# Kernel optimization log

Measured on AMD Instinct MI355X. Metric: run time of the kernel, lower is better.

The kernel has to match this reference:

```python
import jax, jax.numpy as jnp
import numpy as np

B, S, D, H, E = 4, 2048, 2048, 4096, 8
TOP_K = 2
ENTROPY_WEIGHT = 0.1
MAX_USAGE_RATIO = 0.3


def setup_inputs() -> dict:
    key = jax.random.key(0)
    k0, k1, k2 = jax.random.split(key, 3)
    x = jax.random.normal(k0, (B, S, D), dtype=jnp.float32)
    gate_w = jax.random.normal(k1, (E, D), dtype=jnp.float32) * 0.02
    gate_b = jnp.zeros((E,), dtype=jnp.float32)
    expert_w = jax.random.normal(k2, (E, H, D), dtype=jnp.float32) * 0.02
    expert_b = jnp.zeros((E, H), dtype=jnp.float32)
    return {"x": x, "gate_w": gate_w, "gate_b": gate_b,
            "expert_w": expert_w, "expert_b": expert_b}


def reference(x, gate_w, gate_b, expert_w, expert_b):
    b, s, d = x.shape
    e, h, _ = expert_w.shape
    n = b * s
    xf = x.reshape(n, d)

    # gating
    gate_logits = xf @ gate_w.T + gate_b              # (N, E)
    gate_probs = jax.nn.softmax(gate_logits, axis=-1)
    entropy = (-jnp.sum(gate_probs * jnp.log(gate_probs + 1e-10), axis=-1)).mean()
    entropy_loss = ENTROPY_WEIGHT * entropy

    # top-k dispatch weights
    topk_probs, topk_idx = jax.lax.top_k(gate_probs, TOP_K)   # (N, K)
    combine = jnp.sum(jax.nn.one_hot(topk_idx, e, dtype=xf.dtype)
                      * topk_probs[..., None], axis=1)        # (N, E)

    # per-expert linear + weighted combine (loop over small fixed E)
    out = jnp.zeros((n, h), dtype=xf.dtype)
    for ei in range(e):
        out = out + combine[:, ei:ei + 1] * (xf @ expert_w[ei].T + expert_b[ei])

    # usage penalty (this batch's routing counts)
    counts = jnp.sum(jax.nn.one_hot(topk_idx, e, dtype=jnp.float32), axis=(0, 1))
    usage_ratios = counts / n
    overuse_penalty = jnp.sum(jax.nn.relu(usage_ratios - MAX_USAGE_RATIO))

    return out.reshape(b, s, h), entropy_loss + overuse_penalty
```

## Files before the change

### kernel.cpp

```cpp
#include <hip/hip_runtime.h>

constexpr int N_TOK = 8192;
constexpr int D_IN  = 2048;
constexpr int H_OUT = 4096;
constexpr int NEXP  = 8;
constexpr float ENT_W = 0.1f;
constexpr float MAX_USAGE = 0.3f;

constexpr int TM = 128;
constexpr int TH = 128;
constexpr int BK = 32;
constexpr int NKT = D_IN / BK;
constexpr int TILES_H = H_OUT / TH;
constexpr int TM_MAX  = N_TOK / TM;
constexpr int REGION  = 8192;
constexpr int BUFSZ   = TM * BK;

typedef __attribute__((ext_vector_type(8))) short bf16x8;
typedef __attribute__((ext_vector_type(4))) float f32x4;

__device__ __forceinline__ short f2bf(float f) {
    unsigned u = __float_as_uint(f);
    u += 0x7FFF + ((u >> 16) & 1);
    return (short)(u >> 16);
}

__device__ __forceinline__ void gload16(const void* g, void* l) {
    __builtin_amdgcn_global_load_lds(
        (const __attribute__((address_space(1))) unsigned int*)g,
        (__attribute__((address_space(3))) unsigned int*)l, 16, 0, 0);
}

__global__ __launch_bounds__(256) void cvt_kernel(
    const float* __restrict__ in, short* __restrict__ out, int n8)
{
    int stride = gridDim.x * 256;
    for (int i = blockIdx.x * 256 + threadIdx.x; i < n8; i += stride) {
        const float4* p = (const float4*)in + (size_t)i * 2;
        float4 a = p[0], b = p[1];
        bf16x8 v;
        v[0] = f2bf(a.x); v[1] = f2bf(a.y); v[2] = f2bf(a.z); v[3] = f2bf(a.w);
        v[4] = f2bf(b.x); v[5] = f2bf(b.y); v[6] = f2bf(b.z); v[7] = f2bf(b.w);
        *(bf16x8*)(out + (size_t)i * 8) = v;
    }
}

__global__ __launch_bounds__(256) void gate_kernel(
    const float* __restrict__ x, const float* __restrict__ gate_w,
    const float* __restrict__ gate_b, int* __restrict__ topk_idx,
    float* __restrict__ topk_w, float* __restrict__ ent_partial,
    short* __restrict__ xb)
{
    __shared__ float ent_s[4];
    const int wv = threadIdx.x >> 6;
    const int lane = threadIdx.x & 63;
    const int t = blockIdx.x * 4 + wv;

    float acc[NEXP];
#pragma unroll
    for (int e = 0; e < NEXP; ++e) acc[e] = 0.f;

    const float4* xr = (const float4*)(x + (size_t)t * D_IN);
    short* xbr = xb + (size_t)t * D_IN;
#pragma unroll
    for (int i = 0; i < D_IN / 256; ++i) {
        float4 xv = xr[lane + i * 64];
        short4 s4;
        s4.x = f2bf(xv.x); s4.y = f2bf(xv.y); s4.z = f2bf(xv.z); s4.w = f2bf(xv.w);
        *(short4*)(xbr + i * 256 + lane * 4) = s4;
#pragma unroll
        for (int e = 0; e < NEXP; ++e) {
            float4 gv = ((const float4*)(gate_w + e * D_IN))[lane + i * 64];
            acc[e] += xv.x * gv.x + xv.y * gv.y + xv.z * gv.z + xv.w * gv.w;
        }
    }
#pragma unroll
    for (int e = 0; e < NEXP; ++e)
#pragma unroll
        for (int m = 32; m >= 1; m >>= 1) acc[e] += __shfl_xor(acc[e], m, 64);

    if (lane == 0) {
        float lg[NEXP], p[NEXP];
        float mx = -1e30f;
#pragma unroll
        for (int e = 0; e < NEXP; ++e) { lg[e] = acc[e] + gate_b[e]; mx = fmaxf(mx, lg[e]); }
        float s = 0.f;
#pragma unroll
        for (int e = 0; e < NEXP; ++e) { p[e] = expf(lg[e] - mx); s += p[e]; }
        float inv = 1.f / s;
        float ent = 0.f;
#pragma unroll
        for (int e = 0; e < NEXP; ++e) { p[e] *= inv; ent -= p[e] * logf(p[e] + 1e-10f); }
        int e1 = 0; float b1 = p[0];
#pragma unroll
        for (int e = 1; e < NEXP; ++e) if (p[e] > b1) { b1 = p[e]; e1 = e; }
        int e2 = (e1 == 0) ? 1 : 0; float b2 = p[e2];
#pragma unroll
        for (int e = 0; e < NEXP; ++e)
            if (e != e1 && e != ((e1 == 0) ? 1 : 0) && p[e] > b2) { b2 = p[e]; e2 = e; }
        topk_idx[2 * t]     = e1;  topk_idx[2 * t + 1] = e2;
        topk_w[2 * t]       = b1;  topk_w[2 * t + 1]   = b2;
        ent_s[wv] = ent;
    }
    __syncthreads();
    if (threadIdx.x == 0)
        ent_partial[blockIdx.x] = ent_s[0] + ent_s[1] + ent_s[2] + ent_s[3];
}

__global__ __launch_bounds__(256) void scatter_kernel(
    const int* __restrict__ topk_idx, const float* __restrict__ topk_w,
    int* __restrict__ cursors, int* __restrict__ tok_list,
    float* __restrict__ w_list)
{
    __shared__ int lcnt[NEXP], lbase[NEXP];
    const int tid = threadIdx.x;
    const int t = blockIdx.x * 256 + tid;
    if (tid < NEXP) lcnt[tid] = 0;
    __syncthreads();
    int e0 = topk_idx[2 * t], e1 = topk_idx[2 * t + 1];
    float w0 = topk_w[2 * t], w1 = topk_w[2 * t + 1];
    int p0 = atomicAdd(&lcnt[e0], 1);
    int p1 = atomicAdd(&lcnt[e1], 1);
    __syncthreads();
    if (tid < NEXP) lbase[tid] = atomicAdd(&cursors[tid], lcnt[tid]);
    __syncthreads();
    int d0 = e0 * REGION + lbase[e0] + p0;
    int d1 = e1 * REGION + lbase[e1] + p1;
    tok_list[d0] = t;  w_list[d0] = w0;
    tok_list[d1] = t;  w_list[d1] = w1;
}

__global__ __launch_bounds__(256) void finalize_kernel(
    const int* __restrict__ counts, const float* __restrict__ ent_partial,
    float* __restrict__ loss_out)
{
    __shared__ float red[256];
    float s = 0.f;
    for (int i = threadIdx.x; i < N_TOK / 4; i += 256) s += ent_partial[i];
    red[threadIdx.x] = s;
    __syncthreads();
    for (int st = 128; st > 0; st >>= 1) {
        if (threadIdx.x < st) red[threadIdx.x] += red[threadIdx.x + st];
        __syncthreads();
    }
    if (threadIdx.x == 0) {
        float loss = ENT_W * red[0] / (float)N_TOK;
        for (int e = 0; e < NEXP; ++e) {
            float r = (float)counts[e] / (float)N_TOK - MAX_USAGE;
            if (r > 0.f) loss += r;
        }
        loss_out[0] = loss;
    }
}

__global__ __launch_bounds__(256, 4) void moe_gemm(
    const short* __restrict__ xb, const short* __restrict__ wb,
    const float* __restrict__ expert_b, const int* __restrict__ tok_list,
    const float* __restrict__ w_list, const int* __restrict__ counts,
    float* __restrict__ out)
{
    const int bid = blockIdx.x;
    const int e   = bid / (TM_MAX * TILES_H);
    const int rem = bid % (TM_MAX * TILES_H);
    const int tm  = rem / TILES_H;
    const int th  = rem % TILES_H;

    const int cnt = counts[e];
    if (tm * TM >= cnt) return;
    const int valid = cnt - tm * TM;
    const int hbase = th * TH;

    __shared__ __align__(16) short A_s[2][BUFSZ];
    __shared__ __align__(16) short B_s[2][BUFSZ];
    __shared__ int   tok_s[TM];
    __shared__ float wgt_s[TM];

    const int tid = threadIdx.x;
    if (tid < TM) {
        bool v = tid < valid;
        int src = e * REGION + tm * TM + tid;
        tok_s[tid] = v ? tok_list[src] : 0;
        wgt_s[tid] = v ? w_list[src] : 0.f;
    }
    __syncthreads();

    const int lane = tid & 63;
    const int wv = tid >> 6;

    const char* asrc[2];
    const char* bsrc[2];
    int dst_off[2];
#pragma unroll
    for (int j = 0; j < 2; ++j) {
        int c = wv * 2 + j;
        int r = c * 16 + (lane >> 2);
        int s2 = (lane & 3) ^ ((lane >> 3) & 3);
        asrc[j] = (const char*)(xb + (size_t)tok_s[r] * D_IN) + s2 * 16;
        bsrc[j] = (const char*)(wb + ((size_t)e * H_OUT + hbase + r) * D_IN) + s2 * 16;
        dst_off[j] = c * 512;
    }

    const int rr = lane & 15, kg = lane >> 4;
    const int wr = wv >> 1, wc = wv & 1;

    int aoff[4], boff[4];
#pragma unroll
    for (int mi = 0; mi < 4; ++mi) {
        int row = wr * 64 + mi * 16 + rr;
        aoff[mi] = row * 32 + (kg ^ ((row >> 1) & 3)) * 8;
        int rowb = wc * 64 + mi * 16 + rr;
        boff[mi] = rowb * 32 + (kg ^ ((rowb >> 1) & 3)) * 8;
    }

    f32x4 acc[4][4] = {};

#pragma unroll
    for (int j = 0; j < 2; ++j) {
        gload16(asrc[j], (short*)A_s[0] + dst_off[j]); asrc[j] += BK * 2;
        gload16(bsrc[j], (short*)B_s[0] + dst_off[j]); bsrc[j] += BK * 2;
    }
#pragma unroll
    for (int j = 0; j < 2; ++j) {
        gload16(asrc[j], (short*)A_s[1] + dst_off[j]); asrc[j] += BK * 2;
        gload16(bsrc[j], (short*)B_s[1] + dst_off[j]); bsrc[j] += BK * 2;
    }
    asm volatile("s_waitcnt vmcnt(4)" ::: "memory");
    __builtin_amdgcn_sched_barrier(0);
    __builtin_amdgcn_s_barrier();

    for (int kt = 0; kt < NKT; ++kt) {
        const short* Ac = A_s[kt & 1];
        const short* Bc = B_s[kt & 1];
        short* An = (short*)A_s[kt & 1];
        short* Bn = (short*)B_s[kt & 1];

        bf16x8 af[4], bv[4];
#pragma unroll
        for (int mi = 0; mi < 4; ++mi) af[mi] = *(const bf16x8*)&Ac[aoff[mi]];
#pragma unroll
        for (int ni = 0; ni < 4; ++ni) bv[ni] = *(const bf16x8*)&Bc[boff[ni]];
        asm volatile("s_waitcnt lgkmcnt(0)" ::: "memory");
        __builtin_amdgcn_sched_barrier(0);
        __builtin_amdgcn_s_barrier();

        if (kt + 2 < NKT) {
#pragma unroll
            for (int j = 0; j < 2; ++j) {
                gload16(asrc[j], An + dst_off[j]); asrc[j] += BK * 2;
                gload16(bsrc[j], Bn + dst_off[j]); bsrc[j] += BK * 2;
            }
        }

        __builtin_amdgcn_s_setprio(1);
#pragma unroll
        for (int mi = 0; mi < 4; ++mi)
#pragma unroll
            for (int ni = 0; ni < 4; ++ni)
                acc[mi][ni] = __builtin_amdgcn_mfma_f32_16x16x32_bf16(
                    af[mi], bv[ni], acc[mi][ni], 0, 0, 0);
        __builtin_amdgcn_s_setprio(0);

        if (kt + 2 < NKT) {
            asm volatile("s_waitcnt vmcnt(4)" ::: "memory");
        } else if (kt + 1 < NKT) {
            asm volatile("s_waitcnt vmcnt(0)" ::: "memory");
        }
        __builtin_amdgcn_sched_barrier(0);
        __builtin_amdgcn_s_barrier();
    }

    const float* bias = expert_b + (size_t)e * H_OUT + hbase;
#pragma unroll
    for (int mi = 0; mi < 4; ++mi) {
#pragma unroll
        for (int ni = 0; ni < 4; ++ni) {
            int col = wc * 64 + ni * 16 + rr;
            float be = bias[col];
#pragma unroll
            for (int i = 0; i < 4; ++i) {
                int r = wr * 64 + mi * 16 + kg * 4 + i;
                if (r < valid) {
                    float val = wgt_s[r] * (acc[mi][ni][i] + be);
                    atomicAdd(&out[(size_t)tok_s[r] * H_OUT + hbase + col], val);
                }
            }
        }
    }
}

extern "C" void kernel_launch(void* const* d_in, const int* in_sizes, int n_in,
                              void* d_out, int out_size, void* d_ws, size_t ws_size,
                              hipStream_t stream) {
    const float* x        = (const float*)d_in[0];
    const float* gate_w   = (const float*)d_in[1];
    const float* gate_b   = (const float*)d_in[2];
    const float* expert_w = (const float*)d_in[3];
    const float* expert_b = (const float*)d_in[4];
    float* out = (float*)d_out;
    char* ws = (char*)d_ws;

    int*   topk_idx    = (int*)(ws);
    float* topk_w      = (float*)(ws + (64 << 10));
    int*   cursors     = (int*)(ws + (128 << 10));
    float* ent_partial = (float*)(ws + (128 << 10) + 256);
    int*   tok_list    = (int*)(ws + (160 << 10));
    float* w_list      = (float*)(ws + (416 << 10));
    short* xb          = (short*)(ws + (1ull << 20));
    short* wb          = (short*)(ws + (34ull << 20));

    hipMemsetAsync(cursors, 0, 64, stream);
    hipMemsetAsync(d_out, 0, (size_t)out_size * sizeof(float), stream);

    gate_kernel<<<N_TOK / 4, 256, 0, stream>>>(x, gate_w, gate_b, topk_idx,
                                               topk_w, ent_partial, xb);
    cvt_kernel<<<4096, 256, 0, stream>>>(expert_w, wb, (NEXP * H_OUT * D_IN) / 8);
    scatter_kernel<<<N_TOK / 256, 256, 0, stream>>>(topk_idx, topk_w, cursors,
                                                    tok_list, w_list);
    finalize_kernel<<<1, 256, 0, stream>>>(cursors, ent_partial,
                                           out + (size_t)N_TOK * H_OUT);
    moe_gemm<<<NEXP * TM_MAX * TILES_H, 256, 0, stream>>>(
        xb, wb, expert_b, tok_list, w_list, cursors, out);
}
```

Before: 665.0 us.

## Enlarge MoE GEMM tile to 256x128x64 with 512 threads and triple-buffered LDS

```diff
diff --git a/kernel.cpp b/kernel.cpp
--- a/kernel.cpp
+++ b/kernel.cpp
@@ -7,14 +7,15 @@
 constexpr float ENT_W = 0.1f;
 constexpr float MAX_USAGE = 0.3f;
 
-constexpr int TM = 128;
-constexpr int TH = 128;
-constexpr int BK = 32;
+constexpr int BM = 256;
+constexpr int BN = 128;
+constexpr int BK = 64;
 constexpr int NKT = D_IN / BK;
-constexpr int TILES_H = H_OUT / TH;
-constexpr int TM_MAX  = N_TOK / TM;
+constexpr int TILES_H = H_OUT / BN;
+constexpr int TILES_M = N_TOK / BM;
 constexpr int REGION  = 8192;
-constexpr int BUFSZ   = TM * BK;
+constexpr int ASLOT = BM * BK;
+constexpr int BSLOT = BN * BK;
 
 typedef __attribute__((ext_vector_type(8))) short bf16x8;
 typedef __attribute__((ext_vector_type(4))) float f32x4;
@@ -153,32 +154,32 @@
     }
 }
 
-__global__ __launch_bounds__(256, 4) void moe_gemm(
+__global__ __launch_bounds__(512) void moe_gemm(
     const short* __restrict__ xb, const short* __restrict__ wb,
     const float* __restrict__ expert_b, const int* __restrict__ tok_list,
     const float* __restrict__ w_list, const int* __restrict__ counts,
     float* __restrict__ out)
 {
     const int bid = blockIdx.x;
-    const int e   = bid / (TM_MAX * TILES_H);
-    const int rem = bid % (TM_MAX * TILES_H);
+    const int e   = bid / (TILES_M * TILES_H);
+    const int rem = bid % (TILES_M * TILES_H);
     const int tm  = rem / TILES_H;
     const int th  = rem % TILES_H;
 
     const int cnt = counts[e];
-    if (tm * TM >= cnt) return;
-    const int valid = cnt - tm * TM;
-    const int hbase = th * TH;
-
-    __shared__ __align__(16) short A_s[2][BUFSZ];
-    __shared__ __align__(16) short B_s[2][BUFSZ];
-    __shared__ int   tok_s[TM];
-    __shared__ float wgt_s[TM];
+    if (tm * BM >= cnt) return;
+    const int valid = cnt - tm * BM;
+    const int hbase = th * BN;
+
+    __shared__ __align__(16) short A3[3 * ASLOT];
+    __shared__ __align__(16) short B3[3 * BSLOT];
+    __shared__ int   tok_s[BM];
+    __shared__ float wgt_s[BM];
 
     const int tid = threadIdx.x;
-    if (tid < TM) {
+    if (tid < BM) {
         bool v = tid < valid;
-        int src = e * REGION + tm * TM + tid;
+        int src = e * REGION + tm * BM + tid;
         tok_s[tid] = v ? tok_list[src] : 0;
         wgt_s[tid] = v ? w_list[src] : 0.f;
     }
@@ -186,99 +187,132 @@
 
     const int lane = tid & 63;
     const int wv = tid >> 6;
-
-    const char* asrc[2];
-    const char* bsrc[2];
-    int dst_off[2];
-#pragma unroll
-    for (int j = 0; j < 2; ++j) {
-        int c = wv * 2 + j;
-        int r = c * 16 + (lane >> 2);
-        int s2 = (lane & 3) ^ ((lane >> 3) & 3);
-        asrc[j] = (const char*)(xb + (size_t)tok_s[r] * D_IN) + s2 * 16;
-        bsrc[j] = (const char*)(wb + ((size_t)e * H_OUT + hbase + r) * D_IN) + s2 * 16;
-        dst_off[j] = c * 512;
-    }
-
+    const int wm = wv >> 1;
+    const int wn = wv & 1;
     const int rr = lane & 15, kg = lane >> 4;
-    const int wr = wv >> 1, wc = wv & 1;
-
-    int aoff[4], boff[4];
-#pragma unroll
-    for (int mi = 0; mi < 4; ++mi) {
-        int row = wr * 64 + mi * 16 + rr;
-        aoff[mi] = row * 32 + (kg ^ ((row >> 1) & 3)) * 8;
-        int rowb = wc * 64 + mi * 16 + rr;
-        boff[mi] = rowb * 32 + (kg ^ ((rowb >> 1) & 3)) * 8;
-    }
+
+    const char* a_src[2][2];
+    const char* b_src[2];
+    int a_dst[2][2];
+    int b_dst[2];
+#pragma unroll
+    for (int ro = 0; ro < 2; ++ro) {
+        int f = ro * 512 + tid;
+        int row = f >> 3;
+        int s2 = (f & 7) ^ (row & 7);
+#pragma unroll
+        for (int h = 0; h < 2; ++h) {
+            a_src[h][ro] = (const char*)(xb + (size_t)tok_s[h * 128 + row] * D_IN)
+                           + s2 * 16;
+            a_dst[h][ro] = h * 8192 + (ro * 512 + wv * 64) * 8;
+        }
+        b_src[ro] = (const char*)(wb + ((size_t)e * H_OUT + hbase + row) * D_IN)
+                    + s2 * 16;
+        b_dst[ro] = (ro * 512 + wv * 64) * 8;
+    }
+
+    const int Abase = (wm * 64 + rr) * 64;
+    const int Bbase = (wn * 64 + rr) * 64;
+    const int swz0 = (kg ^ (rr & 7)) * 8;
+    const int swz1 = ((4 + kg) ^ (rr & 7)) * 8;
 
     f32x4 acc[4][4] = {};
 
-#pragma unroll
-    for (int j = 0; j < 2; ++j) {
-        gload16(asrc[j], (short*)A_s[0] + dst_off[j]); asrc[j] += BK * 2;
-        gload16(bsrc[j], (short*)B_s[0] + dst_off[j]); bsrc[j] += BK * 2;
-    }
-#pragma unroll
-    for (int j = 0; j < 2; ++j) {
-        gload16(asrc[j], (short*)A_s[1] + dst_off[j]); asrc[j] += BK * 2;
-        gload16(bsrc[j], (short*)B_s[1] + dst_off[j]); bsrc[j] += BK * 2;
-    }
-    asm volatile("s_waitcnt vmcnt(4)" ::: "memory");
+#define STAGE_KT(slot)                                                     \
+    {                                                                      \
+        short* Aso = A3 + (slot) * ASLOT;                                  \
+        short* Bso = B3 + (slot) * BSLOT;                                  \
+        gload16(a_src[0][0], Aso + a_dst[0][0]); a_src[0][0] += 128;       \
+        gload16(a_src[0][1], Aso + a_dst[0][1]); a_src[0][1] += 128;       \
+        gload16(a_src[1][0], Aso + a_dst[1][0]); a_src[1][0] += 128;       \
+        gload16(a_src[1][1], Aso + a_dst[1][1]); a_src[1][1] += 128;       \
+        gload16(b_src[0],    Bso + b_dst[0]);    b_src[0]    += 128;       \
+        gload16(b_src[1],    Bso + b_dst[1]);    b_src[1]    += 128;       \
+    }
+
+    STAGE_KT(0);
+    STAGE_KT(1);
+    asm volatile("s_waitcnt vmcnt(6)" ::: "memory");
     __builtin_amdgcn_sched_barrier(0);
     __builtin_amdgcn_s_barrier();
 
     for (int kt = 0; kt < NKT; ++kt) {
-        const short* Ac = A_s[kt & 1];
-        const short* Bc = B_s[kt & 1];
-        short* An = (short*)A_s[kt & 1];
-        short* Bn = (short*)B_s[kt & 1];
-
-        bf16x8 af[4], bv[4];
-#pragma unroll
-        for (int mi = 0; mi < 4; ++mi) af[mi] = *(const bf16x8*)&Ac[aoff[mi]];
-#pragma unroll
-        for (int ni = 0; ni < 4; ++ni) bv[ni] = *(const bf16x8*)&Bc[boff[ni]];
+        const int slot = kt % 3;
+        const int nslot = (kt + 2) % 3;
+        const short* Ac = A3 + slot * ASLOT;
+        const short* Bc = B3 + slot * BSLOT;
+        const bool pre = (kt + 2 < NKT);
+
+        bf16x8 af[4], bf_[4];
+
+#pragma unroll
+        for (int mi = 0; mi < 4; ++mi)
+            af[mi] = *(const bf16x8*)&Ac[Abase + mi * 1024 + swz0];
+#pragma unroll
+        for (int ni = 0; ni < 4; ++ni)
+            bf_[ni] = *(const bf16x8*)&Bc[Bbase + ni * 1024 + swz0];
+        if (pre) {
+            short* Aso = A3 + nslot * ASLOT;
+            gload16(a_src[0][0], Aso + a_dst[0][0]); a_src[0][0] += 128;
+            gload16(a_src[0][1], Aso + a_dst[0][1]); a_src[0][1] += 128;
+            gload16(a_src[1][0], Aso + a_dst[1][0]); a_src[1][0] += 128;
+            gload16(a_src[1][1], Aso + a_dst[1][1]); a_src[1][1] += 128;
+        }
+        __builtin_amdgcn_s_barrier();
         asm volatile("s_waitcnt lgkmcnt(0)" ::: "memory");
         __builtin_amdgcn_sched_barrier(0);
-        __builtin_amdgcn_s_barrier();
-
-        if (kt + 2 < NKT) {
-#pragma unroll
-            for (int j = 0; j < 2; ++j) {
-                gload16(asrc[j], An + dst_off[j]); asrc[j] += BK * 2;
-                gload16(bsrc[j], Bn + dst_off[j]); bsrc[j] += BK * 2;
-            }
-        }
-
         __builtin_amdgcn_s_setprio(1);
 #pragma unroll
         for (int mi = 0; mi < 4; ++mi)
 #pragma unroll
             for (int ni = 0; ni < 4; ++ni)
                 acc[mi][ni] = __builtin_amdgcn_mfma_f32_16x16x32_bf16(
-                    af[mi], bv[ni], acc[mi][ni], 0, 0, 0);
+                    af[mi], bf_[ni], acc[mi][ni], 0, 0, 0);
         __builtin_amdgcn_s_setprio(0);
-
-        if (kt + 2 < NKT) {
-            asm volatile("s_waitcnt vmcnt(4)" ::: "memory");
+        __builtin_amdgcn_s_barrier();
+
+#pragma unroll
+        for (int mi = 0; mi < 4; ++mi)
+            af[mi] = *(const bf16x8*)&Ac[Abase + mi * 1024 + swz1];
+#pragma unroll
+        for (int ni = 0; ni < 4; ++ni)
+            bf_[ni] = *(const bf16x8*)&Bc[Bbase + ni * 1024 + swz1];
+        if (pre) {
+            short* Bso = B3 + nslot * BSLOT;
+            gload16(b_src[0], Bso + b_dst[0]); b_src[0] += 128;
+            gload16(b_src[1], Bso + b_dst[1]); b_src[1] += 128;
+        }
+        __builtin_amdgcn_s_barrier();
+        asm volatile("s_waitcnt lgkmcnt(0)" ::: "memory");
+        __builtin_amdgcn_sched_barrier(0);
+        __builtin_amdgcn_s_setprio(1);
+#pragma unroll
+        for (int mi = 0; mi < 4; ++mi)
+#pragma unroll
+            for (int ni = 0; ni < 4; ++ni)
+                acc[mi][ni] = __builtin_amdgcn_mfma_f32_16x16x32_bf16(
+                    af[mi], bf_[ni], acc[mi][ni], 0, 0, 0);
+        __builtin_amdgcn_s_setprio(0);
+        if (pre) {
+            asm volatile("s_waitcnt vmcnt(6)" ::: "memory");
         } else if (kt + 1 < NKT) {
             asm volatile("s_waitcnt vmcnt(0)" ::: "memory");
         }
         __builtin_amdgcn_sched_barrier(0);
         __builtin_amdgcn_s_barrier();
     }
+#undef STAGE_KT
 
     const float* bias = expert_b + (size_t)e * H_OUT + hbase;
 #pragma unroll
     for (int mi = 0; mi < 4; ++mi) {
 #pragma unroll
         for (int ni = 0; ni < 4; ++ni) {
-            int col = wc * 64 + ni * 16 + rr;
+            int col = wn * 64 + ni * 16 + rr;
             float be = bias[col];
 #pragma unroll
             for (int i = 0; i < 4; ++i) {
-                int r = wr * 64 + mi * 16 + kg * 4 + i;
+                int r = wm * 64 + mi * 16 + kg * 4 + i;
                 if (r < valid) {
                     float val = wgt_s[r] * (acc[mi][ni][i] + be);
                     atomicAdd(&out[(size_t)tok_s[r] * H_OUT + hbase + col], val);
@@ -318,6 +352,6 @@
                                                     tok_list, w_list);
     finalize_kernel<<<1, 256, 0, stream>>>(cursors, ent_partial,
                                            out + (size_t)N_TOK * H_OUT);
-    moe_gemm<<<NEXP * TM_MAX * TILES_H, 256, 0, stream>>>(
+    moe_gemm<<<NEXP * TILES_M * TILES_H, 512, 0, stream>>>(
         xb, wb, expert_b, tok_list, w_list, cursors, out);
 }
```

Measured after the change: 831.7 us. +25.1%, slower.

## Use triple-buffered LDS to drop mid-iteration barrier in MoE GEMM

Applied to the files above, without the earlier changes.

```diff
diff --git a/kernel.cpp b/kernel.cpp
--- a/kernel.cpp
+++ b/kernel.cpp
@@ -153,7 +153,7 @@
     }
 }
 
-__global__ __launch_bounds__(256, 4) void moe_gemm(
+__global__ __launch_bounds__(256, 3) void moe_gemm(
     const short* __restrict__ xb, const short* __restrict__ wb,
     const float* __restrict__ expert_b, const int* __restrict__ tok_list,
     const float* __restrict__ w_list, const int* __restrict__ counts,
@@ -170,8 +170,8 @@
     const int valid = cnt - tm * TM;
     const int hbase = th * TH;
 
-    __shared__ __align__(16) short A_s[2][BUFSZ];
-    __shared__ __align__(16) short B_s[2][BUFSZ];
+    __shared__ __align__(16) short A_s[3][BUFSZ];
+    __shared__ __align__(16) short B_s[3][BUFSZ];
     __shared__ int   tok_s[TM];
     __shared__ float wgt_s[TM];
 
@@ -214,25 +214,30 @@
 
     f32x4 acc[4][4] = {};
 
-#pragma unroll
-    for (int j = 0; j < 2; ++j) {
-        gload16(asrc[j], (short*)A_s[0] + dst_off[j]); asrc[j] += BK * 2;
-        gload16(bsrc[j], (short*)B_s[0] + dst_off[j]); bsrc[j] += BK * 2;
-    }
-#pragma unroll
-    for (int j = 0; j < 2; ++j) {
-        gload16(asrc[j], (short*)A_s[1] + dst_off[j]); asrc[j] += BK * 2;
-        gload16(bsrc[j], (short*)B_s[1] + dst_off[j]); bsrc[j] += BK * 2;
-    }
+#define STAGE_KT(slot)                                                     \
+    {                                                                      \
+        short* Aso = (short*)A_s[slot];                                    \
+        short* Bso = (short*)B_s[slot];                                    \
+        gload16(asrc[0], Aso + dst_off[0]); asrc[0] += BK * 2;             \
+        gload16(bsrc[0], Bso + dst_off[0]); bsrc[0] += BK * 2;             \
+        gload16(asrc[1], Aso + dst_off[1]); asrc[1] += BK * 2;             \
+        gload16(bsrc[1], Bso + dst_off[1]); bsrc[1] += BK * 2;             \
+    }
+
+    STAGE_KT(0);
+    STAGE_KT(1);
     asm volatile("s_waitcnt vmcnt(4)" ::: "memory");
     __builtin_amdgcn_sched_barrier(0);
     __builtin_amdgcn_s_barrier();
 
     for (int kt = 0; kt < NKT; ++kt) {
-        const short* Ac = A_s[kt & 1];
-        const short* Bc = B_s[kt & 1];
-        short* An = (short*)A_s[kt & 1];
-        short* Bn = (short*)B_s[kt & 1];
+        const int slot = kt % 3;
+        const int nslot = (kt + 2) % 3;
+        const short* Ac = A_s[slot];
+        const short* Bc = B_s[slot];
+        const bool pre = (kt + 2 < NKT);
+
+        if (pre) STAGE_KT(nslot);
 
         bf16x8 af[4], bv[4];
 #pragma unroll
@@ -241,15 +246,6 @@
         for (int ni = 0; ni < 4; ++ni) bv[ni] = *(const bf16x8*)&Bc[boff[ni]];
         asm volatile("s_waitcnt lgkmcnt(0)" ::: "memory");
         __builtin_amdgcn_sched_barrier(0);
-        __builtin_amdgcn_s_barrier();
-
-        if (kt + 2 < NKT) {
-#pragma unroll
-            for (int j = 0; j < 2; ++j) {
-                gload16(asrc[j], An + dst_off[j]); asrc[j] += BK * 2;
-                gload16(bsrc[j], Bn + dst_off[j]); bsrc[j] += BK * 2;
-            }
-        }
 
         __builtin_amdgcn_s_setprio(1);
 #pragma unroll
@@ -260,7 +256,7 @@
                     af[mi], bv[ni], acc[mi][ni], 0, 0, 0);
         __builtin_amdgcn_s_setprio(0);
 
-        if (kt + 2 < NKT) {
+        if (pre) {
             asm volatile("s_waitcnt vmcnt(4)" ::: "memory");
         } else if (kt + 1 < NKT) {
             asm volatile("s_waitcnt vmcnt(0)" ::: "memory");
@@ -268,6 +264,7 @@
         __builtin_amdgcn_sched_barrier(0);
         __builtin_amdgcn_s_barrier();
     }
+#undef STAGE_KT
 
     const float* bias = expert_b + (size_t)e * H_OUT + hbase;
 #pragma unroll
```

Result: slower. 704.1 us (+5.9%).
